# Kernel optimization log

Measured on AMD Instinct MI355X. Metric: run time of the kernel, lower is better.

The kernel has to match this reference:

```python
import jax, jax.numpy as jnp
import numpy as np

N = 50000       # nodes
E = 800000      # edges (avg degree 16)
IN_DIM = 128
H_DIM = 96      # conv='SKP' -> h_dim unchanged
OUT_DIM = 64
NUM_LAYERS = 4
HEADS = 2       # conv='SKP' -> num_heads forced to 2


def setup_inputs() -> dict:
    key = jax.random.key(0)
    ks = jax.random.split(key, 9)
    x = jax.random.normal(ks[0], (N, IN_DIM), jnp.float32)
    edge_index = jax.random.randint(ks[1], (2, E), 0, N, dtype=jnp.int32)
    enc_w = jax.random.normal(ks[2], (IN_DIM, H_DIM), jnp.float32) / np.sqrt(IN_DIM)
    enc_b = jnp.zeros((H_DIM,), jnp.float32)
    dec_w = jax.random.normal(ks[3], (H_DIM, OUT_DIM), jnp.float32) / np.sqrt(H_DIM)
    dec_b = jnp.zeros((OUT_DIM,), jnp.float32)
    # per-layer, per-head linear transforms of the SKP conv
    conv_W = jax.random.normal(ks[4], (NUM_LAYERS, HEADS, H_DIM, H_DIM), jnp.float32) / np.sqrt(H_DIM)
    # per-layer, per-head learnable edge weights (SKP takes num_edges at init)
    conv_ew = jax.random.normal(ks[5], (NUM_LAYERS, HEADS, E), jnp.float32) * 0.1
    return {"x": x, "edge_index": edge_index, "enc_w": enc_w, "enc_b": enc_b,
            "dec_w": dec_w, "dec_b": dec_b, "conv_W": conv_W, "conv_ew": conv_ew}


def _skp_conv(h, src, dst, W, ew):
    # h: [N, d], W: [H, d, d], ew: [H, E]
    # X' = sum_h S_h X W_h  (S_h = learned edge-weighted sparse propagation)
    m = jnp.einsum('nd,hde->hne', h, W)          # [H, N, d] per-head transform
    g = m[:, src, :]                              # [H, E, d] gather at source nodes
    comb = jnp.einsum('he,hed->ed', ew, g)        # weight per edge, sum heads -> [E, d]
    return jax.ops.segment_sum(comb, dst, num_segments=N)  # scatter-add to dest


def reference(x, edge_index, enc_w, enc_b, dec_w, dec_b, conv_W, conv_ew):
    src, dst = edge_index[0], edge_index[1]
    h = jax.nn.relu(x @ enc_w + enc_b)
    for l in range(NUM_LAYERS):
        h = _skp_conv(h, src, dst, conv_W[l], conv_ew[l])
        h = jax.nn.relu(h)   # act=True
    return (h @ dec_w + dec_b, h)
```

## Files before the change

### kernel.cpp

```cpp
#include <hip/hip_runtime.h>

constexpr int IND = 128;
constexpr int HD  = 96;
constexpr int OD  = 64;
constexpr int NL  = 4;

struct F3 { float x, y, z; };

__global__ __launch_bounds__(256) void k_hist(const int* __restrict__ dst, int* __restrict__ deg, int E) {
    int e = blockIdx.x * 256 + threadIdx.x;
    if (e < E) atomicAdd(&deg[dst[e]], 1);
}

__global__ __launch_bounds__(256) void k_scan1(const int* __restrict__ deg, int* __restrict__ bsum, int n) {
    int tid = threadIdx.x;
    int base = blockIdx.x * 1024 + tid * 4;
    int s = 0;
    #pragma unroll
    for (int q = 0; q < 4; ++q) { int i = base + q; if (i < n) s += deg[i]; }
    #pragma unroll
    for (int o = 32; o > 0; o >>= 1) s += __shfl_xor(s, o);
    __shared__ int wsum[4];
    int lane = tid & 63, wid = tid >> 6;
    if (lane == 0) wsum[wid] = s;
    __syncthreads();
    if (tid == 0) bsum[blockIdx.x] = wsum[0] + wsum[1] + wsum[2] + wsum[3];
}

__global__ void k_scan2(const int* __restrict__ bsum, int* __restrict__ boff, int nb,
                        int* __restrict__ row_ptr, int n, int E) {
    int l = threadIdx.x;
    int v = (l < nb) ? bsum[l] : 0;
    int incl = v;
    #pragma unroll
    for (int o = 1; o < 64; o <<= 1) { int t = __shfl_up(incl, o); if (l >= o) incl += t; }
    if (l < nb) boff[l] = incl - v;
    if (l == 0) row_ptr[n] = E;
}

__global__ __launch_bounds__(256) void k_scan3(const int* __restrict__ deg, const int* __restrict__ boff,
                                               int* __restrict__ row_ptr, int n) {
    int tid = threadIdx.x;
    int base = blockIdx.x * 1024 + tid * 4;
    int d[4];
    #pragma unroll
    for (int q = 0; q < 4; ++q) { int i = base + q; d[q] = (i < n) ? deg[i] : 0; }
    int tsum = d[0] + d[1] + d[2] + d[3];
    int incl = tsum;
    #pragma unroll
    for (int o = 1; o < 64; o <<= 1) { int t = __shfl_up(incl, o); if ((tid & 63) >= o) incl += t; }
    __shared__ int wsum[4];
    int lane = tid & 63, wid = tid >> 6;
    if (lane == 63) wsum[wid] = incl;
    __syncthreads();
    int woff = 0;
    for (int w = 0; w < wid; ++w) woff += wsum[w];
    int run = boff[blockIdx.x] + woff + (incl - tsum);
    #pragma unroll
    for (int q = 0; q < 4; ++q) {
        int i = base + q;
        if (i < n) { row_ptr[i] = run; run += d[q]; }
    }
}

__global__ __launch_bounds__(256) void k_fill(const int* __restrict__ src, const int* __restrict__ dst,
                                              const int* __restrict__ row_ptr, int* __restrict__ cursor,
                                              const float* __restrict__ convE,
                                              int* __restrict__ srcp, float2* __restrict__ ewp, int E) {
    int e = blockIdx.x * 256 + threadIdx.x;
    if (e >= E) return;
    int d = dst[e];
    int pos = atomicAdd(&cursor[d], 1);
    int slot = row_ptr[d] + pos;
    srcp[slot] = src[e];
    #pragma unroll
    for (int l = 0; l < NL; ++l) {
        float2 w;
        w.x = convE[(size_t)(2 * l)     * E + e];
        w.y = convE[(size_t)(2 * l + 1) * E + e];
        ewp[(size_t)l * E + slot] = w;
    }
}

constexpr int BR = 32;

__global__ __launch_bounds__(256) void k_layer(const float* __restrict__ hin,
                                               const int* __restrict__ row_ptr,
                                               const int* __restrict__ srcp,
                                               const float2* __restrict__ ewp,
                                               const float* __restrict__ W,
                                               float* __restrict__ hout, int n) {
    __shared__ float sA0[BR][HD];
    __shared__ float sA1[BR][HD];
    int tid = threadIdx.x;
    int brow = blockIdx.x * BR;

    {
        int grp = tid >> 5;
        int lane = tid & 31;
        int off = lane * 3;
        for (int q = 0; q < 4; ++q) {
            int r = grp * 4 + q;
            int g = brow + r;
            float a0x = 0.f, a0y = 0.f, a0z = 0.f;
            float a1x = 0.f, a1y = 0.f, a1z = 0.f;
            if (g < n) {
                int i = row_ptr[g], end = row_ptr[g + 1];
                for (; i + 2 <= end; i += 2) {
                    int s0 = srcp[i];
                    int s1 = srcp[i + 1];
                    float2 w0 = ewp[i];
                    float2 w1 = ewp[i + 1];
                    F3 v0 = *(const F3*)(hin + (size_t)s0 * HD + off);
                    F3 v1 = *(const F3*)(hin + (size_t)s1 * HD + off);
                    a0x = fmaf(w0.x, v0.x, a0x); a0y = fmaf(w0.x, v0.y, a0y); a0z = fmaf(w0.x, v0.z, a0z);
                    a1x = fmaf(w0.y, v0.x, a1x); a1y = fmaf(w0.y, v0.y, a1y); a1z = fmaf(w0.y, v0.z, a1z);
                    a0x = fmaf(w1.x, v1.x, a0x); a0y = fmaf(w1.x, v1.y, a0y); a0z = fmaf(w1.x, v1.z, a0z);
                    a1x = fmaf(w1.y, v1.x, a1x); a1y = fmaf(w1.y, v1.y, a1y); a1z = fmaf(w1.y, v1.z, a1z);
                }
                if (i < end) {
                    int s0 = srcp[i];
                    float2 w0 = ewp[i];
                    F3 v0 = *(const F3*)(hin + (size_t)s0 * HD + off);
                    a0x = fmaf(w0.x, v0.x, a0x); a0y = fmaf(w0.x, v0.y, a0y); a0z = fmaf(w0.x, v0.z, a0z);
                    a1x = fmaf(w0.y, v0.x, a1x); a1y = fmaf(w0.y, v0.y, a1y); a1z = fmaf(w0.y, v0.z, a1z);
                }
            }
            sA0[r][off] = a0x; sA0[r][off + 1] = a0y; sA0[r][off + 2] = a0z;
            sA1[r][off] = a1x; sA1[r][off + 1] = a1y; sA1[r][off + 2] = a1z;
        }
    }
    __syncthreads();

    int tx = tid & 31;
    int ty = tid >> 5;
    float acc[4][3];
    #pragma unroll
    for (int r = 0; r < 4; ++r) { acc[r][0] = 0.f; acc[r][1] = 0.f; acc[r][2] = 0.f; }

    #pragma unroll
    for (int head = 0; head < 2; ++head) {
        const float* Wh = W + (size_t)head * HD * HD;
        const float (*sAh)[HD] = head ? sA1 : sA0;
        #pragma unroll 4
        for (int kk = 0; kk < HD; ++kk) {
            F3 wv = *(const F3*)(Wh + (size_t)kk * HD + 3 * tx);
            float a[4];
            #pragma unroll
            for (int r = 0; r < 4; ++r) a[r] = sAh[4 * ty + r][kk];
            #pragma unroll
            for (int r = 0; r < 4; ++r) {
                acc[r][0] = fmaf(a[r], wv.x, acc[r][0]);
                acc[r][1] = fmaf(a[r], wv.y, acc[r][1]);
                acc[r][2] = fmaf(a[r], wv.z, acc[r][2]);
            }
        }
    }
    #pragma unroll
    for (int r = 0; r < 4; ++r) {
        int gr = brow + 4 * ty + r;
        if (gr < n) {
            float* op = hout + (size_t)gr * HD + 3 * tx;
            op[0] = fmaxf(acc[r][0], 0.f);
            op[1] = fmaxf(acc[r][1], 0.f);
            op[2] = fmaxf(acc[r][2], 0.f);
        }
    }
}

template<int K, int NO, bool RELU>
__global__ __launch_bounds__(256) void k_mlp(const float* __restrict__ A,
                                             const float* __restrict__ W,
                                             const float* __restrict__ bias,
                                             float* __restrict__ out, int n) {
    constexpr int P = K + 4;
    constexpr int NC = NO / 32;
    __shared__ float sA[64][P];
    int tid = threadIdx.x;
    int brow = blockIdx.x * 64;
    constexpr int F4 = K / 4;
    for (int i = tid; i < 64 * F4; i += 256) {
        int r = i / F4, c4 = i % F4;
        int gr = brow + r;
        float4 v = make_float4(0.f, 0.f, 0.f, 0.f);
        if (gr < n) v = *(const float4*)(A + (size_t)gr * K + 4 * c4);
        *(float4*)&sA[r][4 * c4] = v;
    }
    __syncthreads();
    int tx = tid & 31;
    int ty = tid >> 5;
    float acc[8][NC];
    #pragma unroll
    for (int r = 0; r < 8; ++r)
        #pragma unroll
        for (int j = 0; j < NC; ++j) acc[r][j] = 0.f;
    #pragma unroll 4
    for (int kk = 0; kk < K; ++kk) {
        float wv[NC];
        #pragma unroll
        for (int j = 0; j < NC; ++j) wv[j] = W[(size_t)kk * NO + NC * tx + j];
        float a[8];
        #pragma unroll
        for (int r = 0; r < 8; ++r) a[r] = sA[8 * ty + r][kk];
        #pragma unroll
        for (int r = 0; r < 8; ++r)
            #pragma unroll
            for (int j = 0; j < NC; ++j) acc[r][j] = fmaf(a[r], wv[j], acc[r][j]);
    }
    #pragma unroll
    for (int r = 0; r < 8; ++r) {
        int gr = brow + 8 * ty + r;
        if (gr < n) {
            float* op = out + (size_t)gr * NO + NC * tx;
            #pragma unroll
            for (int j = 0; j < NC; ++j) {
                float v = acc[r][j] + bias[NC * tx + j];
                if (RELU) v = fmaxf(v, 0.f);
                op[j] = v;
            }
        }
    }
}

extern "C" void kernel_launch(void* const* d_in, const int* in_sizes, int n_in,
                              void* d_out, int out_size, void* d_ws, size_t ws_size,
                              hipStream_t stream) {
    const float* x     = (const float*)d_in[0];
    const int*   ei    = (const int*)  d_in[1];
    const float* enc_w = (const float*)d_in[2];
    const float* enc_b = (const float*)d_in[3];
    const float* dec_w = (const float*)d_in[4];
    const float* dec_b = (const float*)d_in[5];
    const float* convW = (const float*)d_in[6];
    const float* convE = (const float*)d_in[7];

    const int N = in_sizes[0] / IND;
    const int E = in_sizes[1] / 2;
    const int* src = ei;
    const int* dst = ei + E;
    float* fout = (float*)d_out;

    char* wp = (char*)d_ws;
    auto carve = [&](size_t bytes) -> void* {
        void* p = (void*)wp;
        wp += (bytes + 255) & ~(size_t)255;
        return p;
    };
    int*    deg     = (int*)carve(2 * (size_t)N * 4);
    int*    cursor  = deg + N;
    int*    row_ptr = (int*)carve(((size_t)N + 1) * 4);
    int*    bsum    = (int*)carve(64 * 4);
    int*    boff    = (int*)carve(64 * 4);
    int*    srcp    = (int*)carve((size_t)E * 4);
    float2* ewp     = (float2*)carve((size_t)NL * E * 8);
    float*  hbuf    = (float*)carve((size_t)N * HD * 4);

    hipMemsetAsync(deg, 0, 2 * (size_t)N * 4, stream);

    int ebl = (E + 255) / 256;
    int nb  = (N + 1023) / 1024;
    k_hist<<<ebl, 256, 0, stream>>>(dst, deg, E);
    k_scan1<<<nb, 256, 0, stream>>>(deg, bsum, N);
    k_scan2<<<1, 64, 0, stream>>>(bsum, boff, nb, row_ptr, N, E);
    k_scan3<<<nb, 256, 0, stream>>>(deg, boff, row_ptr, N);
    k_fill<<<ebl, 256, 0, stream>>>(src, dst, row_ptr, cursor, convE, srcp, ewp, E);

    int gbl64 = (N + 63) / 64;
    int gbl32 = (N + BR - 1) / BR;
    float* hfin = fout + (size_t)N * OD;

    k_mlp<IND, HD, true><<<gbl64, 256, 0, stream>>>(x, enc_w, enc_b, hfin, N);

    float* bufs[2] = { hfin, hbuf };
    for (int l = 0; l < NL; ++l) {
        const float* Wl = convW + (size_t)l * 2 * HD * HD;
        const float* hi = bufs[l & 1];
        float*       ho = bufs[(l + 1) & 1];
        k_layer<<<gbl32, 256, 0, stream>>>(hi, row_ptr, srcp, ewp + (size_t)l * E, Wl, ho, N);
    }
    k_mlp<HD, OD, false><<<gbl64, 256, 0, stream>>>(hfin, dec_w, dec_b, fout, N);
}
```

Before: 687.3 us.

## Split edge fill into permutation pass and halve layer row tile

```diff
diff --git a/kernel.cpp b/kernel.cpp
--- a/kernel.cpp
+++ b/kernel.cpp
@@ -65,28 +65,34 @@
 
 __global__ __launch_bounds__(256) void k_fill(const int* __restrict__ src, const int* __restrict__ dst,
                                               const int* __restrict__ row_ptr, int* __restrict__ cursor,
-                                              const float* __restrict__ convE,
-                                              int* __restrict__ srcp, float2* __restrict__ ewp, int E) {
+                                              int2* __restrict__ sep, int E) {
     int e = blockIdx.x * 256 + threadIdx.x;
     if (e >= E) return;
     int d = dst[e];
     int pos = atomicAdd(&cursor[d], 1);
-    int slot = row_ptr[d] + pos;
-    srcp[slot] = src[e];
+    sep[row_ptr[d] + pos] = make_int2(src[e], e);
+}
+
+__global__ __launch_bounds__(256) void k_perm(const int2* __restrict__ sep,
+                                              const float* __restrict__ convE,
+                                              float2* __restrict__ ewp, int E) {
+    int i = blockIdx.x * 256 + threadIdx.x;
+    if (i >= E) return;
+    int e = sep[i].y;
     #pragma unroll
     for (int l = 0; l < NL; ++l) {
         float2 w;
         w.x = convE[(size_t)(2 * l)     * E + e];
         w.y = convE[(size_t)(2 * l + 1) * E + e];
-        ewp[(size_t)l * E + slot] = w;
-    }
-}
-
-constexpr int BR = 32;
+        ewp[(size_t)l * E + i] = w;
+    }
+}
+
+constexpr int BR = 16;
 
 __global__ __launch_bounds__(256) void k_layer(const float* __restrict__ hin,
                                                const int* __restrict__ row_ptr,
-                                               const int* __restrict__ srcp,
+                                               const int2* __restrict__ sep,
                                                const float2* __restrict__ ewp,
                                                const float* __restrict__ W,
                                                float* __restrict__ hout, int n) {
@@ -99,16 +105,16 @@
         int grp = tid >> 5;
         int lane = tid & 31;
         int off = lane * 3;
-        for (int q = 0; q < 4; ++q) {
-            int r = grp * 4 + q;
+        for (int q = 0; q < 2; ++q) {
+            int r = grp * 2 + q;
             int g = brow + r;
             float a0x = 0.f, a0y = 0.f, a0z = 0.f;
             float a1x = 0.f, a1y = 0.f, a1z = 0.f;
             if (g < n) {
                 int i = row_ptr[g], end = row_ptr[g + 1];
                 for (; i + 2 <= end; i += 2) {
-                    int s0 = srcp[i];
-                    int s1 = srcp[i + 1];
+                    int s0 = sep[i].x;
+                    int s1 = sep[i + 1].x;
                     float2 w0 = ewp[i];
                     float2 w1 = ewp[i + 1];
                     F3 v0 = *(const F3*)(hin + (size_t)s0 * HD + off);
@@ -119,7 +125,7 @@
                     a1x = fmaf(w1.y, v1.x, a1x); a1y = fmaf(w1.y, v1.y, a1y); a1z = fmaf(w1.y, v1.z, a1z);
                 }
                 if (i < end) {
-                    int s0 = srcp[i];
+                    int s0 = sep[i].x;
                     float2 w0 = ewp[i];
                     F3 v0 = *(const F3*)(hin + (size_t)s0 * HD + off);
                     a0x = fmaf(w0.x, v0.x, a0x); a0y = fmaf(w0.x, v0.y, a0y); a0z = fmaf(w0.x, v0.z, a0z);
@@ -134,9 +140,9 @@
 
     int tx = tid & 31;
     int ty = tid >> 5;
-    float acc[4][3];
-    #pragma unroll
-    for (int r = 0; r < 4; ++r) { acc[r][0] = 0.f; acc[r][1] = 0.f; acc[r][2] = 0.f; }
+    float acc[2][3];
+    #pragma unroll
+    for (int r = 0; r < 2; ++r) { acc[r][0] = 0.f; acc[r][1] = 0.f; acc[r][2] = 0.f; }
 
     #pragma unroll
     for (int head = 0; head < 2; ++head) {
@@ -145,11 +151,11 @@
         #pragma unroll 4
         for (int kk = 0; kk < HD; ++kk) {
             F3 wv = *(const F3*)(Wh + (size_t)kk * HD + 3 * tx);
-            float a[4];
-            #pragma unroll
-            for (int r = 0; r < 4; ++r) a[r] = sAh[4 * ty + r][kk];
-            #pragma unroll
-            for (int r = 0; r < 4; ++r) {
+            float a[2];
+            #pragma unroll
+            for (int r = 0; r < 2; ++r) a[r] = sAh[2 * ty + r][kk];
+            #pragma unroll
+            for (int r = 0; r < 2; ++r) {
                 acc[r][0] = fmaf(a[r], wv.x, acc[r][0]);
                 acc[r][1] = fmaf(a[r], wv.y, acc[r][1]);
                 acc[r][2] = fmaf(a[r], wv.z, acc[r][2]);
@@ -157,8 +163,8 @@
         }
     }
     #pragma unroll
-    for (int r = 0; r < 4; ++r) {
-        int gr = brow + 4 * ty + r;
+    for (int r = 0; r < 2; ++r) {
+        int gr = brow + 2 * ty + r;
         if (gr < n) {
             float* op = hout + (size_t)gr * HD + 3 * tx;
             op[0] = fmaxf(acc[r][0], 0.f);
@@ -251,7 +257,7 @@
     int*    row_ptr = (int*)carve(((size_t)N + 1) * 4);
     int*    bsum    = (int*)carve(64 * 4);
     int*    boff    = (int*)carve(64 * 4);
-    int*    srcp    = (int*)carve((size_t)E * 4);
+    int2*   sep     = (int2*)carve((size_t)E * 8);
     float2* ewp     = (float2*)carve((size_t)NL * E * 8);
     float*  hbuf    = (float*)carve((size_t)N * HD * 4);
 
@@ -263,10 +269,11 @@
     k_scan1<<<nb, 256, 0, stream>>>(deg, bsum, N);
     k_scan2<<<1, 64, 0, stream>>>(bsum, boff, nb, row_ptr, N, E);
     k_scan3<<<nb, 256, 0, stream>>>(deg, boff, row_ptr, N);
-    k_fill<<<ebl, 256, 0, stream>>>(src, dst, row_ptr, cursor, convE, srcp, ewp, E);
+    k_fill<<<ebl, 256, 0, stream>>>(src, dst, row_ptr, cursor, sep, E);
+    k_perm<<<ebl, 256, 0, stream>>>(sep, convE, ewp, E);
 
     int gbl64 = (N + 63) / 64;
-    int gbl32 = (N + BR - 1) / BR;
+    int gblBR = (N + BR - 1) / BR;
     float* hfin = fout + (size_t)N * OD;
 
     k_mlp<IND, HD, true><<<gbl64, 256, 0, stream>>>(x, enc_w, enc_b, hfin, N);
@@ -276,7 +283,7 @@
         const float* Wl = convW + (size_t)l * 2 * HD * HD;
         const float* hi = bufs[l & 1];
         float*       ho = bufs[(l + 1) & 1];
-        k_layer<<<gbl32, 256, 0, stream>>>(hi, row_ptr, srcp, ewp + (size_t)l * E, Wl, ho, N);
+        k_layer<<<gblBR, 256, 0, stream>>>(hi, row_ptr, sep, ewp + (size_t)l * E, Wl, ho, N);
     }
     k_mlp<HD, OD, false><<<gbl64, 256, 0, stream>>>(hfin, dec_w, dec_b, fout, N);
 }
```

Result: slower. 773.5 us (+12.5%).
